# Kernel tuning notes

Measured on AMD Instinct MI355X. Metric: run time of the kernel, lower is better.

Reference implementation:

```python
import jax, jax.numpy as jnp
import numpy as np
from jax import lax

B = 2048


def setup_inputs() -> dict:
    key = jax.random.key(0)
    ks = jax.random.split(key, 12)
    r = lambda k, s, sc=0.05: jax.random.normal(k, s, jnp.float32) * sc
    return {
        "w": jax.random.normal(ks[0], (B, 512), jnp.float32),
        "init_const": r(ks[1], (1, 512, 4, 4), 0.1),
        "init_conv_w": r(ks[2], (256, 512, 3, 3)),
        "init_conv_b": r(ks[3], (256,)),
        "aff1_w": r(ks[4], (256, 512)),
        "aff1_b": r(ks[5], (256,)),
        "conv1_w": r(ks[6], (128, 256, 3, 3)),
        "conv1_b": r(ks[7], (128,)),
        "aff2_w": r(ks[8], (128, 512)),
        "aff2_b": r(ks[9], (128,)),
        "conv2_w": r(ks[10], (64, 128, 3, 3)),
        "conv2_b": r(ks[11], (64,)),
    }


def _conv3(x, W):
    # 3x3 conv, stride 1, padding 1, NCHW / OIHW
    return lax.conv_general_dilated(x, W, (1, 1), ((1, 1), (1, 1)),
                                    dimension_numbers=("NCHW", "OIHW", "NCHW"))


def _lrelu(x):
    return jnp.where(x >= 0, x, 0.2 * x)


def reference(w, init_const, init_conv_w, init_conv_b,
              aff1_w, aff1_b, conv1_w, conv1_b,
              aff2_w, aff2_b, conv2_w, conv2_b):
    batch = w.shape[0]
    x = _conv3(init_const, init_conv_w) + init_conv_b[None, :, None, None]
    x = _lrelu(x)                                   # [1,256,4,4]
    x = jnp.broadcast_to(x, (batch,) + x.shape[1:])  # repeat over batch
    layers = ((aff1_w, aff1_b, conv1_w, conv1_b),
              (aff2_w, aff2_b, conv2_w, conv2_b))
    for aw, ab, cw, cb in layers:
        b_, c, h, wd = x.shape
        # bilinear upsample x2 (half-pixel centers == torch align_corners=False)
        x = jax.image.resize(x, (b_, c, 2 * h, 2 * wd), "bilinear")
        style = w @ aw.T + ab                        # [B, Cin]
        # modulated conv: conv(s*x, W) * demod, where
        # demod[b,o] = rsqrt(sum_{c,k} (s[b,c] W[o,c,k])^2 + 1e-8)
        xm = x * style[:, :, None, None]
        y = _conv3(xm, cw)                           # [B, Cout, 2h, 2w]
        w2 = jnp.sum(cw * cw, axis=(2, 3))           # [Cout, Cin]
        demod = lax.rsqrt(jnp.einsum("bc,oc->bo", style * style, w2) + 1e-8)
        x = _lrelu(y * demod[:, :, None, None] + cb[None, :, None, None])
    return x
```

## Files before the change

### kernel.cpp

```cpp
#include <hip/hip_runtime.h>
#include <hip/hip_fp16.h>

typedef _Float16 f16x8 __attribute__((ext_vector_type(8)));
typedef float f32x4 __attribute__((ext_vector_type(4)));

#define WS_X0U   0
#define WS_GHP   65536
#define WS_W2P   4259840
#define WS_WH    4407296
#define WS_AFTH  6504448
#define WS_W2TH  6897664
#define WS_S1P   7045120
#define WS_S2H   8093696
#define WS_SSQ   8617984
#define WS_D1    10190848
#define WS_D2    11239424
#define WS_X1T   11763712

__device__ __forceinline__ void up_wi(int j, int S, int& i0, int& i1,
                                      float& w0, float& w1) {
  int m = j >> 1;
  if (j & 1) { i0 = m; i1 = (m + 1 < S) ? m + 1 : S - 1; w0 = 0.75f; w1 = 0.25f; }
  else       { i0 = (m - 1 >= 0) ? m - 1 : 0; i1 = m;     w0 = 0.25f; w1 = 0.75f; }
}

__device__ __forceinline__ int xq_off(int pix, int i) {
  return (pix >> 1) * 64 + (((((pix & 1) << 2) + i) ^ ((pix >> 1) & 7)) << 3);
}

__global__ __launch_bounds__(256) void k_init(const float* __restrict__ ic,
    const float* __restrict__ w0c, const float* __restrict__ b0,
    float* __restrict__ x0u) {
  int o = blockIdx.x, t = threadIdx.x;
  int pix = t & 15, cg = t >> 4;
  int py = pix >> 2, px = pix & 3;
  __shared__ float part[16][17];
  __shared__ float x4[16];
  float acc = 0.f;
  int c0 = cg * 32;
  for (int c = c0; c < c0 + 32; ++c) {
    const float* wp = w0c + (o * 512 + c) * 9;
    const float* xp = ic + c * 16;
#pragma unroll
    for (int dy = 0; dy < 3; ++dy) {
      int iy = py + dy - 1;
      if ((unsigned)iy >= 4u) continue;
#pragma unroll
      for (int dx = 0; dx < 3; ++dx) {
        int ix = px + dx - 1;
        if ((unsigned)ix >= 4u) continue;
        acc += wp[dy * 3 + dx] * xp[iy * 4 + ix];
      }
    }
  }
  part[cg][pix] = acc;
  __syncthreads();
  if (t < 16) {
    float v = b0[o];
#pragma unroll
    for (int g = 0; g < 16; ++g) v += part[g][t];
    x4[t] = (v >= 0.f) ? v : 0.2f * v;
  }
  __syncthreads();
  if (t < 64) {
    int oy = t >> 3, ox = t & 7;
    int y0, y1, xx0, xx1; float wy0, wy1, wx0, wx1;
    up_wi(oy, 4, y0, y1, wy0, wy1);
    up_wi(ox, 4, xx0, xx1, wx0, wx1);
    float v = wy0 * (wx0 * x4[y0 * 4 + xx0] + wx1 * x4[y0 * 4 + xx1])
            + wy1 * (wx0 * x4[y1 * 4 + xx0] + wx1 * x4[y1 * 4 + xx1]);
    x0u[o * 64 + t] = v;
  }
}

__global__ __launch_bounds__(256) void k_prep(const float* __restrict__ w1c,
    const float* __restrict__ x0u, _Float16* __restrict__ Ghp) {
  int o = blockIdx.x, pg = blockIdx.y, t = threadIdx.x;
  __shared__ _Float16 x0l[256][66];
  for (int i = t; i < 256 * 64; i += 256) {
    int c = i >> 6, p = i & 63;
    x0l[c][p] = (_Float16)x0u[i];
  }
  __syncthreads();
  int c = t;
  float wr9[9];
#pragma unroll
  for (int k = 0; k < 9; ++k) wr9[k] = w1c[(o * 256 + c) * 9 + k];
  int cpart = ((((c >> 3) & 3) * 16 + (o & 15)) * 8) + (c & 7);
  int cq = c >> 5, oq = o >> 4;
  for (int p = pg * 16; p < pg * 16 + 16; ++p) {
    int py = p >> 3, px = p & 7;
    float acc = 0.f;
#pragma unroll
    for (int dy = 0; dy < 3; ++dy) {
      int iy = py + dy - 1;
      if ((unsigned)iy >= 8u) continue;
#pragma unroll
      for (int dx = 0; dx < 3; ++dx) {
        int ix = px + dx - 1;
        if ((unsigned)ix >= 8u) continue;
        acc += wr9[dy * 3 + dx] * (float)x0l[c][iy * 8 + ix];
      }
    }
    Ghp[((p * 8 + oq) * 8 + cq) * 512 + cpart] = (_Float16)acc;
  }
}

__global__ __launch_bounds__(256) void k_misc(const float* __restrict__ w1c,
    const float* __restrict__ w2c, const float* __restrict__ a1w,
    const float* __restrict__ a2w, const float* __restrict__ wsrc,
    _Float16* __restrict__ w2p, _Float16* __restrict__ wh,
    _Float16* __restrict__ afTh, _Float16* __restrict__ W2Th) {
  int idx = blockIdx.x * 256 + threadIdx.x;
  if (idx < 73728) {
    int tap = idx / 8192, r = idx & 8191;
    int kg = r >> 11, mf = (r >> 9) & 3, l = (r >> 3) & 63, j = r & 7;
    int o = mf * 16 + (l & 15);
    int c = kg * 32 + (l >> 4) * 8 + j;
    w2p[idx] = (_Float16)w2c[(o * 128 + c) * 9 + tap];
  } else if (idx < 73728 + 1048576) {
    int i = idx - 73728;
    wh[i] = (_Float16)wsrc[i];
  } else if (idx < 73728 + 1048576 + 196608) {
    int i = idx - 73728 - 1048576;
    afTh[i] = (_Float16)((i < 131072) ? a1w[i] : a2w[i - 131072]);
  } else if (idx < 73728 + 1048576 + 196608 + 73728) {
    int i = idx - 73728 - 1048576 - 196608;
    int o = i / 384, k = i - o * 384;
    float v = 0.f;
    const float* wp = nullptr;
    if (o < 128 && k < 256)        wp = w1c + (o * 256 + k) * 9;
    else if (o >= 128 && k >= 256) wp = w2c + ((o - 128) * 128 + (k - 256)) * 9;
    if (wp) {
#pragma unroll
      for (int q = 0; q < 9; ++q) v += wp[q] * wp[q];
    }
    W2Th[i] = (_Float16)v;
  }
}

__global__ __launch_bounds__(256) void k_sty(const _Float16* __restrict__ wh,
    const _Float16* __restrict__ afTh, const float* __restrict__ a1b,
    const float* __restrict__ a2b, _Float16* __restrict__ s1p,
    _Float16* __restrict__ s2h, _Float16* __restrict__ ssq) {
  int t = threadIdx.x, lane = t & 63, w = t >> 6;
  int wr = w >> 1, wc = w & 1;
  int b0 = blockIdx.y * 64 + wr * 32;
  int f0 = blockIdx.x * 64 + wc * 32;
  f32x4 acc[2][2] = {};
  int lr = lane & 15, lk = (lane >> 4) * 8;
#pragma unroll
  for (int kg = 0; kg < 16; ++kg) {
    f16x8 af[2], bf[2];
#pragma unroll
    for (int mf = 0; mf < 2; ++mf)
      af[mf] = *(const f16x8*)(wh + (b0 + mf * 16 + lr) * 512 + kg * 32 + lk);
#pragma unroll
    for (int nf = 0; nf < 2; ++nf)
      bf[nf] = *(const f16x8*)(afTh + (f0 + nf * 16 + lr) * 512 + kg * 32 + lk);
#pragma unroll
    for (int mf = 0; mf < 2; ++mf)
#pragma unroll
      for (int nf = 0; nf < 2; ++nf)
        acc[mf][nf] = __builtin_amdgcn_mfma_f32_16x16x32_f16(af[mf], bf[nf], acc[mf][nf], 0, 0, 0);
  }
  int r4 = lane >> 4;
#pragma unroll
  for (int nf = 0; nf < 2; ++nf) {
    int f = f0 + nf * 16 + lr;
    float bias = (f < 256) ? a1b[f] : a2b[f - 256];
#pragma unroll
    for (int mf = 0; mf < 2; ++mf) {
#pragma unroll
      for (int r = 0; r < 4; ++r) {
        int b = b0 + mf * 16 + r4 * 4 + r;
        float v = acc[mf][nf][r] + bias;
        ssq[b * 384 + f] = (_Float16)(v * v);
        if (f < 256) {
          int flat = (((b >> 4) * 8 + (f >> 5)) * 64 + ((f >> 3) & 3) * 16 + (b & 15)) * 8 + (f & 7);
          s1p[flat] = (_Float16)v;
        } else {
          s2h[b * 128 + (f - 256)] = (_Float16)v;
        }
      }
    }
  }
}

__global__ __launch_bounds__(256) void k_dmd(const _Float16* __restrict__ ssq,
    const _Float16* __restrict__ W2Th, float* __restrict__ d1,
    float* __restrict__ d2) {
  int t = threadIdx.x, lane = t & 63, w = t >> 6;
  int wr = w >> 1, wc = w & 1;
  int b0 = blockIdx.y * 64 + wr * 32;
  int o0 = blockIdx.x * 64 + wc * 32;
  int kbeg = (blockIdx.x == 2) ? 8 : 0;
  int kend = (blockIdx.x == 2) ? 12 : 8;
  f32x4 acc[2][2] = {};
  int lr = lane & 15, lk = (lane >> 4) * 8;
  for (int kg = kbeg; kg < kend; ++kg) {
    f16x8 af[2], bf[2];
#pragma unroll
    for (int mf = 0; mf < 2; ++mf)
      af[mf] = *(const f16x8*)(ssq + (b0 + mf * 16 + lr) * 384 + kg * 32 + lk);
#pragma unroll
    for (int nf = 0; nf < 2; ++nf)
      bf[nf] = *(const f16x8*)(W2Th + (o0 + nf * 16 + lr) * 384 + kg * 32 + lk);
#pragma unroll
    for (int mf = 0; mf < 2; ++mf)
#pragma unroll
      for (int nf = 0; nf < 2; ++nf)
        acc[mf][nf] = __builtin_amdgcn_mfma_f32_16x16x32_f16(af[mf], bf[nf], acc[mf][nf], 0, 0, 0);
  }
  int r4 = lane >> 4;
#pragma unroll
  for (int mf = 0; mf < 2; ++mf) {
#pragma unroll
    for (int r = 0; r < 4; ++r) {
      int b = b0 + mf * 16 + r4 * 4 + r;
#pragma unroll
      for (int nf = 0; nf < 2; ++nf) {
        int o = o0 + nf * 16 + lr;
        float v = rsqrtf(acc[mf][nf][r] + 1e-8f);
        if (o < 128) d1[b * 128 + o] = v;
        else         d2[b * 64 + (o - 128)] = v;
      }
    }
  }
}

__global__ __launch_bounds__(256) void k_l1(const _Float16* __restrict__ s1p,
    const _Float16* __restrict__ Ghp, const float* __restrict__ d1,
    const float* __restrict__ c1b, const _Float16* __restrict__ s2h,
    __half* __restrict__ x1t) {
  int t = threadIdx.x, lane = t & 63, w = t >> 6;
  int wr = w >> 1, wc = w & 1;
  int bq0 = blockIdx.y * 8 + wr * 4;
  int nq0 = blockIdx.x * 8 + wc * 4;
  f32x4 acc[4][4] = {};
#pragma unroll
  for (int kg = 0; kg < 8; ++kg) {
    f16x8 af[4], bf[4];
#pragma unroll
    for (int mf = 0; mf < 4; ++mf)
      af[mf] = *(const f16x8*)(s1p + (((bq0 + mf) * 8 + kg) * 64 + lane) * 8);
#pragma unroll
    for (int nf = 0; nf < 4; ++nf)
      bf[nf] = *(const f16x8*)(Ghp + (((nq0 + nf) * 8 + kg) * 64 + lane) * 8);
#pragma unroll
    for (int mf = 0; mf < 4; ++mf)
#pragma unroll
      for (int nf = 0; nf < 4; ++nf)
        acc[mf][nf] = __builtin_amdgcn_mfma_f32_16x16x32_f16(af[mf], bf[nf], acc[mf][nf], 0, 0, 0);
  }
  int nc = lane & 15, r4 = lane >> 4;
#pragma unroll
  for (int mf = 0; mf < 4; ++mf) {
#pragma unroll
    for (int r = 0; r < 4; ++r) {
      int b = (bq0 + mf) * 16 + r4 * 4 + r;
#pragma unroll
      for (int nf = 0; nf < 4; ++nf) {
        int n = (nq0 + nf) * 16 + nc;
        int o = n & 127, p = n >> 7;
        float v = acc[mf][nf][r] * d1[b * 128 + o] + c1b[o];
        v = (v >= 0.f) ? v : 0.2f * v;
        v *= (float)s2h[b * 128 + o];
        x1t[(b * 64 + p) * 128 + o] = (__half)v;
      }
    }
  }
}

__global__ __launch_bounds__(256, 2) void k_l2(const __half* __restrict__ x1t,
    const float* __restrict__ d2g, const _Float16* __restrict__ w2p,
    const float* __restrict__ c2b, float* __restrict__ out) {
  int b = blockIdx.x, t = threadIdx.x;
  int lane = t & 63, w = t >> 6;
  __shared__ unsigned short xq[2][9792];
  __shared__ unsigned short x1l[64 * 128];
  const __half* xb = x1t + b * 8192;

  for (int idx = t; idx < 1024; idx += 256) {
    int q = idx >> 4, gc = idx & 15;
    f16x8 v = *(const f16x8*)(xb + q * 128 + gc * 8);
    int gs = (gc & 8) | ((gc ^ q) & 7);
    *(f16x8*)&x1l[q * 128 + gs * 8] = v;
  }
  {
    f16x8 z = {};
    for (int idx = t; idx < 400; idx += 256) {
      int pg = idx >> 3, g = idx & 7;
      int buf = g >> 2, i = g & 3;
      int pix;
      if (pg < 18) pix = 288 + pg;
      else { int j = pg - 18; pix = (j >> 1) * 18 + (j & 1) * 17; }
      *(f16x8*)&xq[buf][xq_off(pix, i)] = z;
    }
  }
  f16x8 afb[3][4];
#pragma unroll
  for (int mf = 0; mf < 4; ++mf) {
    afb[0][mf] = *(const f16x8*)(w2p + (((0 * 4 + 0) * 4 + mf) * 64 + lane) * 8);
    afb[1][mf] = *(const f16x8*)(w2p + (((3 * 4 + 0) * 4 + mf) * 64 + lane) * 8);
  }
  int fy = t >> 4, fx = t & 15;
  int y0, y1, x0, x1i; float wy0, wy1, wx0, wx1;
  up_wi(fy, 8, y0, y1, wy0, wy1);
  up_wi(fx, 8, x0, x1i, wx0, wx1);
  _Float16 wA = (_Float16)(wy0 * wx0), wB = (_Float16)(wy0 * wx1);
  _Float16 wC = (_Float16)(wy1 * wx0), wD = (_Float16)(wy1 * wx1);
  int pixb = fy * 18 + fx + 1;
  int q00 = y0 * 8 + x0, q01 = y0 * 8 + x1i, q10 = y1 * 8 + x0, q11 = y1 * 8 + x1i;

  auto build_granule = [&](int qn, int i) {
    int gc = qn * 4 + i;
    f16x8 va = *(const f16x8*)&x1l[q00 * 128 + ((gc & 8) | ((gc ^ q00) & 7)) * 8];
    f16x8 vb = *(const f16x8*)&x1l[q01 * 128 + ((gc & 8) | ((gc ^ q01) & 7)) * 8];
    f16x8 vc = *(const f16x8*)&x1l[q10 * 128 + ((gc & 8) | ((gc ^ q10) & 7)) * 8];
    f16x8 vd = *(const f16x8*)&x1l[q11 * 128 + ((gc & 8) | ((gc ^ q11) & 7)) * 8];
    f16x8 v = va * wA;
    v += vb * wB;
    v += vc * wC;
    v += vd * wD;
    *(f16x8*)&xq[qn & 1][xq_off(pixb, i)] = v;
  };

  __syncthreads();
#pragma unroll
  for (int i = 0; i < 4; ++i) build_granule(0, i);
  __syncthreads();

  f32x4 acc[4][4] = {};
  f16x8 rw[2][6];
  int ig = lane >> 4;
  int colb = lane & 15;

  auto read_win = [&](int qb, int buf, int dx) {
#pragma unroll
    for (int j = 0; j < 6; ++j) {
      int fr = w * 4 + j - 1;
      int srow = ((unsigned)fr < 16u) ? fr : 16;
      int pix = srow * 18 + colb + dx;
      rw[buf][j] = *(const f16x8*)&xq[qb][xq_off(pix, ig)];
    }
  };

#pragma unroll
  for (int q = 0; q < 4; ++q) {
    read_win(q & 1, 0, 0);
#pragma unroll
    for (int dx = 0; dx < 3; ++dx) {
      if (dx < 2) read_win(q & 1, (dx + 1) & 1, dx + 1);
      if (q < 3) {
        if (dx == 0) { build_granule(q + 1, 0); build_granule(q + 1, 1); }
        else if (dx == 1) build_granule(q + 1, 2);
        else              build_granule(q + 1, 3);
      }
#pragma unroll
      for (int dy = 0; dy < 3; ++dy) {
        const int u = q * 9 + dx * 3 + dy;
        if (u + 2 < 36) {
          const int un = u + 2;
          const int qn = un / 9, rn = un - qn * 9;
          const int dxn = rn / 3, dyn = rn - dxn * 3;
          const int tapn = dyn * 3 + dxn;
#pragma unroll
          for (int mf = 0; mf < 4; ++mf)
            afb[un % 3][mf] = *(const f16x8*)(w2p + (((tapn * 4 + qn) * 4 + mf) * 64 + lane) * 8);
        }
        __builtin_amdgcn_s_setprio(1);
#pragma unroll
        for (int mf = 0; mf < 4; ++mf)
#pragma unroll
          for (int nf = 0; nf < 4; ++nf)
            acc[mf][nf] = __builtin_amdgcn_mfma_f32_16x16x32_f16(afb[u % 3][mf], rw[dx & 1][nf + dy], acc[mf][nf], 0, 0, 0);
        __builtin_amdgcn_s_setprio(0);
      }
    }
    if (q < 3) __syncthreads();
  }
  int px = lane & 15, r4 = lane >> 4;
#pragma unroll
  for (int mf = 0; mf < 4; ++mf) {
#pragma unroll
    for (int r = 0; r < 4; ++r) {
      int o = mf * 16 + r4 * 4 + r;
      float dm = d2g[b * 64 + o], bias = c2b[o];
#pragma unroll
      for (int nf = 0; nf < 4; ++nf) {
        int py = w * 4 + nf;
        float v = acc[mf][nf][r] * dm + bias;
        v = (v >= 0.f) ? v : 0.2f * v;
        out[(b * 64 + o) * 256 + py * 16 + px] = v;
      }
    }
  }
}

extern "C" void kernel_launch(void* const* d_in, const int* in_sizes, int n_in,
                              void* d_out, int out_size, void* d_ws, size_t ws_size,
                              hipStream_t stream) {
  const float* w    = (const float*)d_in[0];
  const float* ic   = (const float*)d_in[1];
  const float* w0c  = (const float*)d_in[2];
  const float* b0   = (const float*)d_in[3];
  const float* a1w  = (const float*)d_in[4];
  const float* a1b  = (const float*)d_in[5];
  const float* w1c  = (const float*)d_in[6];
  const float* c1b  = (const float*)d_in[7];
  const float* a2w  = (const float*)d_in[8];
  const float* a2b  = (const float*)d_in[9];
  const float* w2c  = (const float*)d_in[10];
  const float* c2b  = (const float*)d_in[11];
  float* out = (float*)d_out;
  char* ws = (char*)d_ws;

  float*    x0u  = (float*)(ws + WS_X0U);
  _Float16* Ghp  = (_Float16*)(ws + WS_GHP);
  _Float16* w2p  = (_Float16*)(ws + WS_W2P);
  _Float16* wh   = (_Float16*)(ws + WS_WH);
  _Float16* afTh = (_Float16*)(ws + WS_AFTH);
  _Float16* W2Th = (_Float16*)(ws + WS_W2TH);
  _Float16* s1p  = (_Float16*)(ws + WS_S1P);
  _Float16* s2h  = (_Float16*)(ws + WS_S2H);
  _Float16* ssq  = (_Float16*)(ws + WS_SSQ);
  float*    d1   = (float*)(ws + WS_D1);
  float*    d2   = (float*)(ws + WS_D2);
  __half*   x1t  = (__half*)(ws + WS_X1T);

  k_init <<<256, 256, 0, stream>>>(ic, w0c, b0, x0u);
  dim3 gp(128, 4);
  k_prep <<<gp, 256, 0, stream>>>(w1c, x0u, Ghp);
  k_misc <<<5440, 256, 0, stream>>>(w1c, w2c, a1w, a2w, w, w2p, wh, afTh, W2Th);
  dim3 gs(6, 32);
  k_sty  <<<gs, 256, 0, stream>>>(wh, afTh, a1b, a2b, s1p, s2h, ssq);
  dim3 gd(3, 32);
  k_dmd  <<<gd, 256, 0, stream>>>(ssq, W2Th, d1, d2);
  dim3 g1(64, 16);
  k_l1   <<<g1, 256, 0, stream>>>(s1p, Ghp, d1, c1b, s2h, x1t);
  k_l2   <<<2048, 256, 0, stream>>>(x1t, d2, w2p, c2b, out);
}
```

Before: 155.5 us.

## Split layer-2 conv into two half-image blocks per batch to raise occupancy

Each batch image in k_l2 is now processed by two blocks, each covering 8 output rows with a halo. This shrinks shared memory, accumulators, the window registers and the weight prefetch buffer, so launch bounds can move to 4 blocks per CU. The upsample build is spread across threads with per-element index math instead of fixed per-thread weights. In exchange, the halo rows are recomputed, the weight reloads from global double, weight prefetch depth drops from two steps to one, and the build needs more integer work per element.

```diff
diff --git a/kernel.cpp b/kernel.cpp
--- a/kernel.cpp
+++ b/kernel.cpp
@@ -272,109 +272,97 @@
   }
 }
 
-__global__ __launch_bounds__(256, 2) void k_l2(const __half* __restrict__ x1t,
+__global__ __launch_bounds__(256, 4) void k_l2(const __half* __restrict__ x1t,
     const float* __restrict__ d2g, const _Float16* __restrict__ w2p,
     const float* __restrict__ c2b, float* __restrict__ out) {
-  int b = blockIdx.x, t = threadIdx.x;
+  int b = blockIdx.x, h = blockIdx.y, t = threadIdx.x;
   int lane = t & 63, w = t >> 6;
-  __shared__ unsigned short xq[2][9792];
-  __shared__ unsigned short x1l[64 * 128];
+  __shared__ unsigned short xq[2][5760];
+  __shared__ unsigned short x1l[40 * 128];
   const __half* xb = x1t + b * 8192;
-
-  for (int idx = t; idx < 1024; idx += 256) {
-    int q = idx >> 4, gc = idx & 15;
-    f16x8 v = *(const f16x8*)(xb + q * 128 + gc * 8);
-    int gs = (gc & 8) | ((gc ^ q) & 7);
-    *(f16x8*)&x1l[q * 128 + gs * 8] = v;
+  const int cr0 = h ? 3 : 0;
+  const int padlr = h ? 9 : 0;
+
+  for (int idx = t; idx < 640; idx += 256) {
+    int cp = idx >> 4, gc = idx & 15;
+    f16x8 v = *(const f16x8*)(xb + (cr0 * 8 + cp) * 128 + gc * 8);
+    int gs = (gc & 8) | ((gc ^ cp) & 7);
+    *(f16x8*)&x1l[cp * 128 + gs * 8] = v;
   }
   {
     f16x8 z = {};
-    for (int idx = t; idx < 400; idx += 256) {
-      int pg = idx >> 3, g = idx & 7;
-      int buf = g >> 2, i = g & 3;
+    for (int idx = t; idx < 304; idx += 256) {
+      int pg = idx >> 3, gsel = idx & 7;
+      int buf = gsel >> 2, i = gsel & 3;
       int pix;
-      if (pg < 18) pix = 288 + pg;
+      if (pg < 18) pix = padlr * 18 + pg;
       else { int j = pg - 18; pix = (j >> 1) * 18 + (j & 1) * 17; }
       *(f16x8*)&xq[buf][xq_off(pix, i)] = z;
     }
   }
-  f16x8 afb[3][4];
-#pragma unroll
-  for (int mf = 0; mf < 4; ++mf) {
-    afb[0][mf] = *(const f16x8*)(w2p + (((0 * 4 + 0) * 4 + mf) * 64 + lane) * 8);
-    afb[1][mf] = *(const f16x8*)(w2p + (((3 * 4 + 0) * 4 + mf) * 64 + lane) * 8);
-  }
-  int fy = t >> 4, fx = t & 15;
-  int y0, y1, x0, x1i; float wy0, wy1, wx0, wx1;
-  up_wi(fy, 8, y0, y1, wy0, wy1);
-  up_wi(fx, 8, x0, x1i, wx0, wx1);
-  _Float16 wA = (_Float16)(wy0 * wx0), wB = (_Float16)(wy0 * wx1);
-  _Float16 wC = (_Float16)(wy1 * wx0), wD = (_Float16)(wy1 * wx1);
-  int pixb = fy * 18 + fx + 1;
-  int q00 = y0 * 8 + x0, q01 = y0 * 8 + x1i, q10 = y1 * 8 + x0, q11 = y1 * 8 + x1i;
-
-  auto build_granule = [&](int qn, int i) {
+  f16x8 afb[2][4];
+#pragma unroll
+  for (int mf = 0; mf < 4; ++mf)
+    afb[0][mf] = *(const f16x8*)(w2p + ((0 * 4 + mf) * 64 + lane) * 8);
+
+  auto build_one = [&](int qn, int idx) {
+    int i = idx / 144, p = idx - i * 144;
+    int rowr = p >> 4, c = p & 15;
+    int gfr = h ? 7 + rowr : rowr;
+    int y0, y1, x0, x1i; float wy0, wy1, wx0, wx1;
+    up_wi(gfr, 8, y0, y1, wy0, wy1);
+    up_wi(c, 8, x0, x1i, wx0, wx1);
+    int c00 = (y0 - cr0) * 8 + x0, c01 = (y0 - cr0) * 8 + x1i;
+    int c10 = (y1 - cr0) * 8 + x0, c11 = (y1 - cr0) * 8 + x1i;
     int gc = qn * 4 + i;
-    f16x8 va = *(const f16x8*)&x1l[q00 * 128 + ((gc & 8) | ((gc ^ q00) & 7)) * 8];
-    f16x8 vb = *(const f16x8*)&x1l[q01 * 128 + ((gc & 8) | ((gc ^ q01) & 7)) * 8];
-    f16x8 vc = *(const f16x8*)&x1l[q10 * 128 + ((gc & 8) | ((gc ^ q10) & 7)) * 8];
-    f16x8 vd = *(const f16x8*)&x1l[q11 * 128 + ((gc & 8) | ((gc ^ q11) & 7)) * 8];
-    f16x8 v = va * wA;
-    v += vb * wB;
-    v += vc * wC;
-    v += vd * wD;
-    *(f16x8*)&xq[qn & 1][xq_off(pixb, i)] = v;
+    f16x8 va = *(const f16x8*)&x1l[c00 * 128 + ((gc & 8) | ((gc ^ c00) & 7)) * 8];
+    f16x8 vb = *(const f16x8*)&x1l[c01 * 128 + ((gc & 8) | ((gc ^ c01) & 7)) * 8];
+    f16x8 vc = *(const f16x8*)&x1l[c10 * 128 + ((gc & 8) | ((gc ^ c10) & 7)) * 8];
+    f16x8 vd = *(const f16x8*)&x1l[c11 * 128 + ((gc & 8) | ((gc ^ c11) & 7)) * 8];
+    f16x8 v = va * (_Float16)(wy0 * wx0);
+    v += vb * (_Float16)(wy0 * wx1);
+    v += vc * (_Float16)(wy1 * wx0);
+    v += vd * (_Float16)(wy1 * wx1);
+    int lr = rowr + (h ? 0 : 1);
+    *(f16x8*)&xq[qn & 1][xq_off(lr * 18 + c + 1, i)] = v;
   };
 
   __syncthreads();
-#pragma unroll
-  for (int i = 0; i < 4; ++i) build_granule(0, i);
+  for (int idx = t; idx < 576; idx += 256) build_one(0, idx);
   __syncthreads();
 
-  f32x4 acc[4][4] = {};
-  f16x8 rw[2][6];
-  int ig = lane >> 4;
-  int colb = lane & 15;
-
-  auto read_win = [&](int qb, int buf, int dx) {
-#pragma unroll
-    for (int j = 0; j < 6; ++j) {
-      int fr = w * 4 + j - 1;
-      int srow = ((unsigned)fr < 16u) ? fr : 16;
-      int pix = srow * 18 + colb + dx;
-      rw[buf][j] = *(const f16x8*)&xq[qb][xq_off(pix, ig)];
-    }
-  };
+  f32x4 acc[4][2] = {};
+  f16x8 rw[4];
+  int ig = lane >> 4, colb = lane & 15;
 
 #pragma unroll
   for (int q = 0; q < 4; ++q) {
-    read_win(q & 1, 0, 0);
 #pragma unroll
     for (int dx = 0; dx < 3; ++dx) {
-      if (dx < 2) read_win(q & 1, (dx + 1) & 1, dx + 1);
-      if (q < 3) {
-        if (dx == 0) { build_granule(q + 1, 0); build_granule(q + 1, 1); }
-        else if (dx == 1) build_granule(q + 1, 2);
-        else              build_granule(q + 1, 3);
-      }
+#pragma unroll
+      for (int j = 0; j < 4; ++j) {
+        int pix = (w * 2 + j) * 18 + colb + dx;
+        rw[j] = *(const f16x8*)&xq[q & 1][xq_off(pix, ig)];
+      }
+      if (q < 3 && t < 192) build_one(q + 1, dx * 192 + t);
 #pragma unroll
       for (int dy = 0; dy < 3; ++dy) {
         const int u = q * 9 + dx * 3 + dy;
-        if (u + 2 < 36) {
-          const int un = u + 2;
+        if (u + 1 < 36) {
+          const int un = u + 1;
           const int qn = un / 9, rn = un - qn * 9;
           const int dxn = rn / 3, dyn = rn - dxn * 3;
           const int tapn = dyn * 3 + dxn;
 #pragma unroll
           for (int mf = 0; mf < 4; ++mf)
-            afb[un % 3][mf] = *(const f16x8*)(w2p + (((tapn * 4 + qn) * 4 + mf) * 64 + lane) * 8);
+            afb[un & 1][mf] = *(const f16x8*)(w2p + (((tapn * 4 + qn) * 4 + mf) * 64 + lane) * 8);
         }
         __builtin_amdgcn_s_setprio(1);
 #pragma unroll
         for (int mf = 0; mf < 4; ++mf)
 #pragma unroll
-          for (int nf = 0; nf < 4; ++nf)
-            acc[mf][nf] = __builtin_amdgcn_mfma_f32_16x16x32_f16(afb[u % 3][mf], rw[dx & 1][nf + dy], acc[mf][nf], 0, 0, 0);
+          for (int nf = 0; nf < 2; ++nf)
+            acc[mf][nf] = __builtin_amdgcn_mfma_f32_16x16x32_f16(afb[u & 1][mf], rw[nf + dy], acc[mf][nf], 0, 0, 0);
         __builtin_amdgcn_s_setprio(0);
       }
     }
@@ -388,11 +376,11 @@
       int o = mf * 16 + r4 * 4 + r;
       float dm = d2g[b * 64 + o], bias = c2b[o];
 #pragma unroll
-      for (int nf = 0; nf < 4; ++nf) {
-        int py = w * 4 + nf;
+      for (int nf = 0; nf < 2; ++nf) {
+        int gr = h * 8 + w * 2 + nf;
         float v = acc[mf][nf][r] * dm + bias;
         v = (v >= 0.f) ? v : 0.2f * v;
-        out[(b * 64 + o) * 256 + py * 16 + px] = v;
+        out[(b * 64 + o) * 256 + gr * 16 + px] = v;
       }
     }
   }
@@ -439,5 +427,6 @@
   k_dmd  <<<gd, 256, 0, stream>>>(ssq, W2Th, d1, d2);
   dim3 g1(64, 16);
   k_l1   <<<g1, 256, 0, stream>>>(s1p, Ghp, d1, c1b, s2h, x1t);
-  k_l2   <<<2048, 256, 0, stream>>>(x1t, d2, w2p, c2b, out);
-}
+  dim3 gl2(2048, 2);
+  k_l2   <<<gl2, 256, 0, stream>>>(x1t, d2, w2p, c2b, out);
+}
```

After: 178.5 us. 1.15x slower.
